# Performance work log

Hardware: AMD Instinct MI355X
Metric: run time of the kernel (lower is better)

## Reference

```python
import jax, jax.numpy as jnp
import numpy as np

EMB = 1024
HEADS = 16
HEAD_DIM = EMB // HEADS
MASK_VAL = -10000.0


def setup_inputs() -> dict:
    key = jax.random.key(0)
    ks = jax.random.split(key, 5)
    B, S = 4, 2048
    x = jax.random.normal(ks[0], (B, S, EMB), dtype=jnp.float32)
    scale = 1.0 / np.sqrt(EMB)
    w_qkv = jax.random.normal(ks[1], (EMB, 3 * EMB), dtype=jnp.float32) * scale
    b_qkv = jnp.zeros((3 * EMB,), dtype=jnp.float32)
    w_fc = jax.random.normal(ks[2], (EMB, EMB), dtype=jnp.float32) * scale
    b_fc = jnp.zeros((EMB,), dtype=jnp.float32)
    return {"x": x, "w_qkv": w_qkv, "b_qkv": b_qkv, "w_fc": w_fc, "b_fc": b_fc}


def reference(x, w_qkv, b_qkv, w_fc, b_fc):
    B, S, _ = x.shape
    qkv = x @ w_qkv + b_qkv                      # (B, S, 3*EMB)
    q, k, v = jnp.split(qkv, 3, axis=-1)
    # split heads: (B, S, EMB) -> (B, H, S, Dh)
    def sh(t):
        return t.reshape(B, S, HEADS, HEAD_DIM).transpose(0, 2, 1, 3)
    q, k, v = sh(q), sh(k), sh(v)
    scores = jnp.einsum('bhqd,bhkd->bhqk', q, k) / np.sqrt(HEAD_DIM)
    causal = jnp.tril(jnp.ones((S, S), dtype=bool))[None, None]
    scores = jnp.where(causal, scores, jnp.float32(MASK_VAL))
    probs = jax.nn.softmax(scores, axis=-1)
    out = jnp.einsum('bhqk,bhkd->bhqd', probs, v)
    out = out.transpose(0, 2, 1, 3).reshape(B, S, EMB)  # merge heads
    return out @ w_fc + b_fc
```

## Files before the change

kernel.cpp:

```cpp
#include <hip/hip_runtime.h>
#include <hip/hip_bf16.h>
#include <cstdint>

#define BF16 __hip_bfloat16

typedef __attribute__((ext_vector_type(8))) short bhalf8;
typedef __attribute__((ext_vector_type(4))) float floatx4;

#define MFMA16(a, b, c) __builtin_amdgcn_mfma_f32_16x16x32_bf16((a), (b), (c), 0, 0, 0)

#define MASKV (-30000.0f)
#define QSCALE 0.18033688011112042f

__device__ __forceinline__ bhalf8 cvt8(const float* p) {
  const float4 f0 = *(const float4*)p;
  const float4 f1 = *(const float4*)(p + 4);
  union { bhalf8 v; ushort u[8]; } r;
  const float t[8] = {f0.x, f0.y, f0.z, f0.w, f1.x, f1.y, f1.z, f1.w};
#pragma unroll
  for (int i = 0; i < 8; ++i) {
    BF16 h = __float2bfloat16(t[i]);
    r.u[i] = *(const ushort*)&h;
  }
  return r.v;
}

__global__ void cvt_f32_bf16(const float* __restrict__ in, BF16* __restrict__ out) {
  const size_t i = ((size_t)blockIdx.x * 256 + threadIdx.x) * 8;
  *(bhalf8*)(out + i) = cvt8(in + i);
}

__global__ void transpose_cvt(const float* __restrict__ in, ushort* __restrict__ out,
                              int R, int C) {
  __shared__ ushort t[32][33];
  const int c0 = blockIdx.x * 32, r0 = blockIdx.y * 32;
  const int tx = threadIdx.x, ty = threadIdx.y;
#pragma unroll
  for (int j = 0; j < 32; j += 8) {
    BF16 h = __float2bfloat16(in[(size_t)(r0 + ty + j) * C + c0 + tx]);
    t[ty + j][tx] = *(const ushort*)&h;
  }
  __syncthreads();
#pragma unroll
  for (int j = 0; j < 32; j += 8)
    out[(size_t)(c0 + ty + j) * R + r0 + tx] = t[tx][ty + j];
}

template <int MODE>
__global__ __launch_bounds__(256, 2) void gemm_bt(
    const BF16* __restrict__ A, const BF16* __restrict__ Bt, const float* __restrict__ bias,
    void* __restrict__ C0v, BF16* __restrict__ C1, BF16* __restrict__ C2,
    int Md, int Nd, int Kd) {
  __shared__ __align__(16) BF16 As[128 * 64];
  __shared__ __align__(16) BF16 Bs[128 * 64];

  const int tid = threadIdx.x;
  const int w = tid >> 6, lane = tid & 63;
  const int lm = lane & 15, quad = lane >> 4;
  const int wm = (w >> 1) * 64, wn = (w & 1) * 64;

  const int lin = blockIdx.y * gridDim.x + blockIdx.x;
  const int per8 = (gridDim.x * gridDim.y) >> 3;
  const int swz = (lin & 7) * per8 + (lin >> 3);
  const int tile_m = (swz / gridDim.x) * 128, tile_n = (swz % gridDim.x) * 128;

  floatx4 acc[4][4];
#pragma unroll
  for (int i = 0; i < 4; ++i)
#pragma unroll
    for (int j = 0; j < 4; ++j) acc[i][j] = (floatx4){0.f, 0.f, 0.f, 0.f};

  int srow[4], sgs[4], sslot[4];
#pragma unroll
  for (int j = 0; j < 4; ++j) {
    const int slot = (j * 4 + w) * 64 + lane;
    sslot[j] = slot;
    srow[j] = slot >> 3;
    sgs[j] = ((slot & 7) - (slot >> 3)) & 7;
  }

  bhalf8 va[4], vb[4], nva[4], nvb[4];
#pragma unroll
  for (int j = 0; j < 4; ++j) {
    va[j] = *(const bhalf8*)(A + (size_t)(tile_m + srow[j]) * Kd + sgs[j] * 8);
    vb[j] = *(const bhalf8*)(Bt + (size_t)(tile_n + srow[j]) * Kd + sgs[j] * 8);
  }

  for (int k0 = 0; k0 < Kd; k0 += 64) {
    __syncthreads();
#pragma unroll
    for (int j = 0; j < 4; ++j) {
      *(bhalf8*)(As + sslot[j] * 8) = va[j];
      *(bhalf8*)(Bs + sslot[j] * 8) = vb[j];
    }
    __syncthreads();

    if (k0 + 64 < Kd) {
      const int k1 = k0 + 64;
#pragma unroll
      for (int j = 0; j < 4; ++j) {
        nva[j] = *(const bhalf8*)(A + (size_t)(tile_m + srow[j]) * Kd + k1 + sgs[j] * 8);
        nvb[j] = *(const bhalf8*)(Bt + (size_t)(tile_n + srow[j]) * Kd + k1 + sgs[j] * 8);
      }
    }

#pragma unroll
    for (int s = 0; s < 2; ++s) {
      bhalf8 af[4], bfr[4];
#pragma unroll
      for (int mt = 0; mt < 4; ++mt) {
        const int r = wm + mt * 16 + lm;
        const int g = ((s * 4 + quad) + r) & 7;
        af[mt] = *(const bhalf8*)(As + r * 64 + g * 8);
      }
#pragma unroll
      for (int nt = 0; nt < 4; ++nt) {
        const int r = wn + nt * 16 + lm;
        const int g = ((s * 4 + quad) + r) & 7;
        bfr[nt] = *(const bhalf8*)(Bs + r * 64 + g * 8);
      }
#pragma unroll
      for (int mt = 0; mt < 4; ++mt)
#pragma unroll
        for (int nt = 0; nt < 4; ++nt)
          acc[mt][nt] = MFMA16(af[mt], bfr[nt], acc[mt][nt]);
    }
#pragma unroll
    for (int j = 0; j < 4; ++j) { va[j] = nva[j]; vb[j] = nvb[j]; }
  }

#pragma unroll
  for (int nt = 0; nt < 4; ++nt) {
    const int n = tile_n + wn + nt * 16 + lm;
    const float bv = bias[n];
#pragma unroll
    for (int mt = 0; mt < 4; ++mt) {
      const int m0 = tile_m + wm + mt * 16 + quad * 4;
      floatx4 v = acc[mt][nt];
      if (MODE == 0) {
        float* C0f = (float*)C0v;
#pragma unroll
        for (int r = 0; r < 4; ++r)
          C0f[(size_t)(m0 + r) * Nd + n] = v[r] + bv;
      } else {
        const int which = n >> 10;
        const int h = (n >> 6) & 15;
        const int d = n & 63;
        if (which == 2) {
          const int b = m0 >> 11, s0 = m0 & 2047;
          union { ushort4 u4; ushort u[4]; } pk;
#pragma unroll
          for (int r = 0; r < 4; ++r) {
            BF16 hv = __float2bfloat16(v[r] + bv);
            pk.u[r] = *(const ushort*)&hv;
          }
          *(ushort4*)(C2 + ((size_t)((b * 16 + h) * 64 + d)) * 2048 + s0) = pk.u4;
        } else {
          BF16* dst = (which == 0) ? (BF16*)C0v : C1;
          const float sc = (which == 0) ? QSCALE : 1.0f;
#pragma unroll
          for (int r = 0; r < 4; ++r) {
            const int m = m0 + r, b = m >> 11, si = m & 2047;
            dst[((size_t)(b * 16 + h) * 2048 + si) * 64 + d] =
                __float2bfloat16((v[r] + bv) * sc);
          }
        }
      }
    }
  }
}

__global__ __launch_bounds__(256, 2) void flash_attn(
    const BF16* __restrict__ Q, const BF16* __restrict__ Kmat,
    const BF16* __restrict__ VT, BF16* __restrict__ O) {
  __shared__ __align__(16) BF16 Ps[4][4][16 * 64];

  const int tid = threadIdx.x;
  const int w = tid >> 6, lane = tid & 63;
  const int lm = lane & 15, quad = lane >> 4;

  const int bid = blockIdx.x;
  const int xcd = bid & 7;
  const int li = bid >> 3;
  const int bh = xcd * 8 + (li >> 3);
  const int x = li & 7;

  const int qt = (w == 0) ? x : (w == 1) ? (15 - x) : (w == 2) ? (16 + x) : (31 - x);
  const int qb0 = qt * 64;
  const size_t bh_off = (size_t)bh * (2048 * 64);

  bhalf8 aq[4][2];
#pragma unroll
  for (int s2 = 0; s2 < 4; ++s2) {
    const BF16* qp = Q + bh_off + (size_t)(qb0 + s2 * 16 + lm) * 64 + quad * 8;
    aq[s2][0] = *(const bhalf8*)qp;
    aq[s2][1] = *(const bhalf8*)(qp + 32);
  }

  floatx4 oacc[4][4];
  float m_i[4], l_i[4];
#pragma unroll
  for (int s2 = 0; s2 < 4; ++s2) {
    m_i[s2] = MASKV;
    l_i[s2] = 0.f;
#pragma unroll
    for (int i = 0; i < 4; ++i) oacc[s2][i] = (floatx4){0.f, 0.f, 0.f, 0.f};
  }

  for (int kt = 0; kt <= qt; ++kt) {
    const int k0 = kt * 64;

    bhalf8 ak[4][2], av[4][2];
#pragma unroll
    for (int nt = 0; nt < 4; ++nt) {
      const BF16* kp = Kmat + bh_off + (size_t)(k0 + nt * 16 + lm) * 64 + quad * 8;
      ak[nt][0] = *(const bhalf8*)kp;
      ak[nt][1] = *(const bhalf8*)(kp + 32);
      const BF16* vp = VT + bh_off + (size_t)(nt * 16 + lm) * 2048 + k0 + quad * 8;
      av[nt][0] = *(const bhalf8*)vp;
      av[nt][1] = *(const bhalf8*)(vp + 32);
    }

#pragma unroll
    for (int s2 = 0; s2 < 4; ++s2) {
      const int qb = qb0 + s2 * 16;

      floatx4 st[4];
      __builtin_amdgcn_s_setprio(1);
#pragma unroll
      for (int nt = 0; nt < 4; ++nt) {
        floatx4 z = (floatx4){0.f, 0.f, 0.f, 0.f};
        z = MFMA16(ak[nt][0], aq[s2][0], z);
        z = MFMA16(ak[nt][1], aq[s2][1], z);
        st[nt] = z;
      }
      __builtin_amdgcn_s_setprio(0);

      if (k0 + 63 > qb) {
#pragma unroll
        for (int nt = 0; nt < 4; ++nt)
#pragma unroll
          for (int r = 0; r < 4; ++r)
            if ((k0 + nt * 16 + quad * 4 + r) > (qb + lm)) st[nt][r] = MASKV;
      }

      float mx = MASKV;
#pragma unroll
      for (int nt = 0; nt < 4; ++nt)
#pragma unroll
        for (int r = 0; r < 4; ++r) mx = fmaxf(mx, st[nt][r]);
      mx = fmaxf(mx, __shfl_xor(mx, 16, 64));
      mx = fmaxf(mx, __shfl_xor(mx, 32, 64));

      if (!__all(mx <= m_i[s2] + 8.0f)) {
        const float mnew = fmaxf(m_i[s2], mx);
        const float alpha = __builtin_amdgcn_exp2f(m_i[s2] - mnew);
        m_i[s2] = mnew;
        l_i[s2] *= alpha;
#pragma unroll
        for (int dn = 0; dn < 4; ++dn) oacc[s2][dn] *= alpha;
      }

      float rs = 0.f;
#pragma unroll
      for (int nt = 0; nt < 4; ++nt)
#pragma unroll
        for (int r = 0; r < 4; ++r) {
          const float p = __builtin_amdgcn_exp2f(st[nt][r] - m_i[s2]);
          st[nt][r] = p;
          rs += p;
        }

      {
        BF16* pws = Ps[w][s2];
#pragma unroll
        for (int nt = 0; nt < 4; ++nt) {
          union { ushort4 u4; ushort u[4]; } pk;
#pragma unroll
          for (int r = 0; r < 4; ++r) {
            BF16 h = __float2bfloat16(st[nt][r]);
            pk.u[r] = *(const ushort*)&h;
          }
          const int g = ((nt * 2 + (quad >> 1)) + lm) & 7;
          *(ushort4*)(pws + lm * 64 + g * 8 + (quad & 1) * 4) = pk.u4;
        }
      }

      rs += __shfl_xor(rs, 16, 64);
      rs += __shfl_xor(rs, 32, 64);
      l_i[s2] += rs;

      if (s2 > 0) {
        const int sp = s2 - 1;
        const BF16* pwp = Ps[w][sp];
        const bhalf8 ap0 = *(const bhalf8*)(pwp + lm * 64 + ((quad + lm) & 7) * 8);
        const bhalf8 ap1 = *(const bhalf8*)(pwp + lm * 64 + ((4 + quad + lm) & 7) * 8);
        __builtin_amdgcn_s_setprio(1);
#pragma unroll
        for (int dn = 0; dn < 4; ++dn) {
          oacc[sp][dn] = MFMA16(av[dn][0], ap0, oacc[sp][dn]);
          oacc[sp][dn] = MFMA16(av[dn][1], ap1, oacc[sp][dn]);
        }
        __builtin_amdgcn_s_setprio(0);
      }
    }

    {
      const BF16* pwp = Ps[w][3];
      const bhalf8 ap0 = *(const bhalf8*)(pwp + lm * 64 + ((quad + lm) & 7) * 8);
      const bhalf8 ap1 = *(const bhalf8*)(pwp + lm * 64 + ((4 + quad + lm) & 7) * 8);
      __builtin_amdgcn_s_setprio(1);
#pragma unroll
      for (int dn = 0; dn < 4; ++dn) {
        oacc[3][dn] = MFMA16(av[dn][0], ap0, oacc[3][dn]);
        oacc[3][dn] = MFMA16(av[dn][1], ap1, oacc[3][dn]);
      }
      __builtin_amdgcn_s_setprio(0);
    }
  }

  const int b = bh >> 4, h = bh & 15;
#pragma unroll
  for (int s2 = 0; s2 < 4; ++s2) {
    const float inv_l = 1.0f / l_i[s2];
    const size_t orow = (size_t)(b * 2048 + qb0 + s2 * 16 + lm) * 1024 + h * 64;
#pragma unroll
    for (int dn = 0; dn < 4; ++dn) {
      union { ushort4 u4; ushort u[4]; } pk;
#pragma unroll
      for (int r = 0; r < 4; ++r) {
        BF16 h2 = __float2bfloat16(oacc[s2][dn][r] * inv_l);
        pk.u[r] = *(const ushort*)&h2;
      }
      *(ushort4*)(O + orow + dn * 16 + quad * 4) = pk.u4;
    }
  }
}

extern "C" void kernel_launch(void* const* d_in, const int* in_sizes, int n_in,
                              void* d_out, int out_size, void* d_ws, size_t ws_size,
                              hipStream_t stream) {
  const float* x = (const float*)d_in[0];
  const float* w_qkv = (const float*)d_in[1];
  const float* b_qkv = (const float*)d_in[2];
  const float* w_fc = (const float*)d_in[3];
  const float* b_fc = (const float*)d_in[4];
  float* out = (float*)d_out;

  BF16* ws = (BF16*)d_ws;
  BF16* wTqkv = ws;
  BF16* wTfc = wTqkv + 3072 * 1024;
  BF16* xb = wTfc + 1024 * 1024;
  BF16* Qb = xb + 8388608;
  BF16* Kb = Qb + 8388608;
  BF16* VTb = Kb + 8388608;
  BF16* Ob = VTb + 8388608;

  cvt_f32_bf16<<<4096, 256, 0, stream>>>(x, xb);
  transpose_cvt<<<dim3(96, 32), dim3(32, 8), 0, stream>>>(w_qkv, (ushort*)wTqkv, 1024, 3072);
  transpose_cvt<<<dim3(32, 32), dim3(32, 8), 0, stream>>>(w_fc, (ushort*)wTfc, 1024, 1024);

  gemm_bt<1><<<dim3(24, 64), 256, 0, stream>>>(
      xb, wTqkv, b_qkv, (void*)Qb, Kb, VTb, 8192, 3072, 1024);
  flash_attn<<<dim3(512), 256, 0, stream>>>(Qb, Kb, VTb, Ob);
  gemm_bt<0><<<dim3(8, 64), 256, 0, stream>>>(
      Ob, wTfc, b_fc, (void*)out, nullptr, nullptr, 8192, 1024, 1024);
}
```

Baseline: 274.9 us.

## Split each query tile's KV range across two waves and merge partial softmax

Each block now covers two query tiles instead of four. Two waves handle each tile, each taking half of the causal key range, and the grid doubles to 1024 blocks. The second wave writes its partial output accumulators and its row max and row sum to shared memory, and the first wave rescales and combines them before writing the output. This is meant to raise parallelism and shorten the longest per-wave dependency chain, at the cost of extra shared-memory traffic, two block barriers and a combine step.

```diff
diff --git a/kernel.cpp b/kernel.cpp
--- a/kernel.cpp
+++ b/kernel.cpp
@@ -174,6 +174,7 @@
     const BF16* __restrict__ Q, const BF16* __restrict__ Kmat,
     const BF16* __restrict__ VT, BF16* __restrict__ O) {
   __shared__ __align__(16) BF16 Ps[4][4][16 * 64];
+  __shared__ float mlb[2][4][2][16];
 
   const int tid = threadIdx.x;
   const int w = tid >> 6, lane = tid & 63;
@@ -182,11 +183,18 @@
   const int bid = blockIdx.x;
   const int xcd = bid & 7;
   const int li = bid >> 3;
-  const int bh = xcd * 8 + (li >> 3);
-  const int x = li & 7;
-
-  const int qt = (w == 0) ? x : (w == 1) ? (15 - x) : (w == 2) ? (16 + x) : (31 - x);
+  const int bh = xcd * 8 + (li >> 4);
+  const int x = li & 15;
+
+  const int role = (w + x) & 3;
+  const int pair = role >> 1;
+  const int half = role & 1;
+  const int qt = pair ? (31 - x) : x;
   const int qb0 = qt * 64;
+  const int ntk = qt + 1;
+  const int mid = (ntk + 1) >> 1;
+  const int kt_beg = half ? mid : 0;
+  const int kt_end = half ? ntk : mid;
   const size_t bh_off = (size_t)bh * (2048 * 64);
 
   bhalf8 aq[4][2];
@@ -207,7 +215,7 @@
     for (int i = 0; i < 4; ++i) oacc[s2][i] = (floatx4){0.f, 0.f, 0.f, 0.f};
   }
 
-  for (int kt = 0; kt <= qt; ++kt) {
+  for (int kt = kt_beg; kt < kt_end; ++kt) {
     const int k0 = kt * 64;
 
     bhalf8 ak[4][2], av[4][2];
@@ -319,20 +327,45 @@
     }
   }
 
-  const int b = bh >> 4, h = bh & 15;
-#pragma unroll
-  for (int s2 = 0; s2 < 4; ++s2) {
-    const float inv_l = 1.0f / l_i[s2];
-    const size_t orow = (size_t)(b * 2048 + qb0 + s2 * 16 + lm) * 1024 + h * 64;
-#pragma unroll
-    for (int dn = 0; dn < 4; ++dn) {
-      union { ushort4 u4; ushort u[4]; } pk;
-#pragma unroll
-      for (int r = 0; r < 4; ++r) {
-        BF16 h2 = __float2bfloat16(oacc[s2][dn][r] * inv_l);
-        pk.u[r] = *(const ushort*)&h2;
-      }
-      *(ushort4*)(O + orow + dn * 16 + quad * 4) = pk.u4;
+  __syncthreads();
+  float* cb = (float*)(&Ps[pair * 2][0][0]);
+
+  if (half) {
+#pragma unroll
+    for (int s2 = 0; s2 < 4; ++s2) {
+#pragma unroll
+      for (int dn = 0; dn < 4; ++dn)
+        *(floatx4*)&cb[(((s2 << 2) | dn) * 64 + lane) * 4] = oacc[s2][dn];
+      if (quad == 0) {
+        mlb[pair][s2][0][lm] = m_i[s2];
+        mlb[pair][s2][1][lm] = l_i[s2];
+      }
+    }
+  }
+  __syncthreads();
+
+  if (!half) {
+    const int b = bh >> 4, h = bh & 15;
+#pragma unroll
+    for (int s2 = 0; s2 < 4; ++s2) {
+      const float mB = mlb[pair][s2][0][lm];
+      const float lB = mlb[pair][s2][1][lm];
+      const float ms = fmaxf(m_i[s2], mB);
+      const float aA = __builtin_amdgcn_exp2f(m_i[s2] - ms);
+      const float aB = __builtin_amdgcn_exp2f(mB - ms);
+      const float inv_l = 1.0f / (l_i[s2] * aA + lB * aB);
+      const size_t orow = (size_t)(b * 2048 + qb0 + s2 * 16 + lm) * 1024 + h * 64;
+#pragma unroll
+      for (int dn = 0; dn < 4; ++dn) {
+        const floatx4 ob = *(const floatx4*)&cb[(((s2 << 2) | dn) * 64 + lane) * 4];
+        union { ushort4 u4; ushort u[4]; } pk;
+#pragma unroll
+        for (int r = 0; r < 4; ++r) {
+          BF16 h2 = __float2bfloat16((oacc[s2][dn][r] * aA + ob[r] * aB) * inv_l);
+          pk.u[r] = *(const ushort*)&h2;
+        }
+        *(ushort4*)(O + orow + dn * 16 + quad * 4) = pk.u4;
+      }
     }
   }
 }
@@ -362,7 +395,7 @@
 
   gemm_bt<1><<<dim3(24, 64), 256, 0, stream>>>(
       xb, wTqkv, b_qkv, (void*)Qb, Kb, VTb, 8192, 3072, 1024);
-  flash_attn<<<dim3(512), 256, 0, stream>>>(Qb, Kb, VTb, Ob);
+  flash_attn<<<dim3(1024), 256, 0, stream>>>(Qb, Kb, VTb, Ob);
   gemm_bt<0><<<dim3(8, 64), 256, 0, stream>>>(
       Ob, wTfc, b_fc, (void*)out, nullptr, nullptr, 8192, 1024, 1024);
 }
```

New measurement: 281.7 us. 2.5% more time.
